# Kernel optimization log

Measured on AMD Instinct MI355X. Metric: run time of the kernel, lower is better.

## Reference

```python
import jax, jax.numpy as jnp
import numpy as np

B, T, C, H = 2, 1024, 768, 12
D = C // H
HID = 4 * C
EPS_YAT = 1e-6
EPS_LN = 1e-6


def yat_dense(x, kernel, bias, alpha):
    # scale = (sqrt(n_out)/log(1+n_out))**alpha
    y = x @ kernel
    dist = (jnp.sum(x * x, axis=-1, keepdims=True)
            + jnp.sum(kernel * kernel, axis=0) - 2.0 * y)
    y = (y * y) / (dist + EPS_YAT)
    if bias is not None:
        y = y + bias
    n = kernel.shape[1]
    scale = (jnp.sqrt(jnp.float32(n)) / jnp.log1p(jnp.float32(n))) ** alpha
    return y * scale


def layernorm(x, scale):
    mu = jnp.mean(x, axis=-1, keepdims=True)
    var = jnp.mean((x - mu) ** 2, axis=-1, keepdims=True)
    return (x - mu) * jax.lax.rsqrt(var + EPS_LN) * scale


def rope_table(seq_len, dim):
    freqs = jnp.exp(jnp.arange(0, dim, 2, dtype=jnp.float32)
                    * (-jnp.log(10000.0) / dim))
    angles = jnp.arange(seq_len, dtype=jnp.float32)[:, None] * freqs[None, :]
    return jnp.concatenate([jnp.cos(angles), jnp.sin(angles)], axis=-1)  # [T, D]


def block_forward(x, mask, p):
    Bc, Tc, Cc = x.shape
    h = layernorm(x, p['ln1_scale'])
    qkv = yat_dense(h, p['w_qkv'], p['b_qkv'], p['a_qkv'])  # [B,T,3C]
    qkv = qkv.reshape(Bc, Tc, 3, H, D)
    q, k, v = qkv[:, :, 0], qkv[:, :, 1], qkv[:, :, 2]      # [B,T,H,D]
    rope = rope_table(Tc, D)[:, None, :]                     # [T,1,D]
    q = q * rope
    k = k * rope
    scale = 1.0 / jnp.sqrt(jnp.float32(D))
    attn = jnp.einsum('bihd,bjhd->bhij', q, k) * scale       # [B,H,T,T]
    attn = jnp.where(mask, attn, jnp.finfo(attn.dtype).min)
    attn = jax.nn.softmax(attn, axis=-1)
    o = jnp.einsum('bhij,bjhd->bihd', attn, v).reshape(Bc, Tc, Cc)
    o = yat_dense(o, p['w_ao'], p['b_ao'], p['a_ao'])
    x = x + o
    h = layernorm(x, p['ln2_scale'])
    gate = yat_dense(h, p['w_fc'], p['b_fc'], p['a_fc'])
    u = yat_dense(h, p['w_gate'], p['b_gate'], p['a_gate'])
    u = jax.nn.gelu(u) * gate
    u = yat_dense(u, p['w_proj'], p['b_proj'], p['a_proj'])
    return x + u


def setup_inputs() -> dict:
    key = jax.random.key(0)
    ks = jax.random.split(key, 8)
    x = jax.random.normal(ks[0], (B, T, C), dtype=jnp.float32)
    mask = jnp.tril(jnp.ones((T, T), dtype=bool))[None, None]  # causal [1,1,T,T]
    w = lambda k, shp: 0.02 * jax.random.normal(k, shp, dtype=jnp.float32)
    return {
        'x': x, 'mask': mask,
        'ln1_scale': jnp.ones((C,), jnp.float32),
        'w_qkv': w(ks[1], (C, 3 * C)), 'b_qkv': jnp.zeros((3 * C,), jnp.float32),
        'a_qkv': jnp.ones((1,), jnp.float32),
        'w_ao': w(ks[2], (C, C)), 'b_ao': jnp.zeros((C,), jnp.float32),
        'a_ao': jnp.ones((1,), jnp.float32),
        'ln2_scale': jnp.ones((C,), jnp.float32),
        'w_fc': w(ks[3], (C, HID)), 'b_fc': jnp.zeros((HID,), jnp.float32),
        'a_fc': jnp.ones((1,), jnp.float32),
        'w_gate': w(ks[4], (C, HID)), 'b_gate': jnp.zeros((HID,), jnp.float32),
        'a_gate': jnp.ones((1,), jnp.float32),
        'w_proj': w(ks[5], (HID, C)), 'b_proj': jnp.zeros((C,), jnp.float32),
        'a_proj': jnp.ones((1,), jnp.float32),
    }


def reference(x, mask, ln1_scale, w_qkv, b_qkv, a_qkv, w_ao, b_ao, a_ao,
              ln2_scale, w_fc, b_fc, a_fc, w_gate, b_gate, a_gate,
              w_proj, b_proj, a_proj):
    p = dict(ln1_scale=ln1_scale, w_qkv=w_qkv, b_qkv=b_qkv, a_qkv=a_qkv,
             w_ao=w_ao, b_ao=b_ao, a_ao=a_ao, ln2_scale=ln2_scale,
             w_fc=w_fc, b_fc=b_fc, a_fc=a_fc, w_gate=w_gate, b_gate=b_gate,
             a_gate=a_gate, w_proj=w_proj, b_proj=b_proj, a_proj=a_proj)
    return block_forward(x, mask, p)
```

## Files before the change

### kernel.cpp

```cpp
#include <hip/hip_runtime.h>
#include <cstdint>

#define DEVFN static __device__ __forceinline__

typedef __bf16 bf16x8 __attribute__((ext_vector_type(8)));
typedef float f32x4 __attribute__((ext_vector_type(4)));
typedef unsigned short us4 __attribute__((ext_vector_type(4)));

DEVFN unsigned short f2bf(float f) {
  unsigned u = __float_as_uint(f);
  u += 0x7fffu + ((u >> 16) & 1u);
  return (unsigned short)(u >> 16);
}
DEVFN float bf2f(unsigned short h) { return __uint_as_float(((unsigned)h) << 16); }
DEVFN void async16(const void* g, void* l) {
  __builtin_amdgcn_global_load_lds((__attribute__((address_space(1))) const void*)g,
                                   (__attribute__((address_space(3))) void*)l, 16, 0, 0);
}
DEVFN float gelu_t(float u) {
  float z = 0.7978845608028654f * (u + 0.044715f * u * u * u);
  float zc = fminf(fmaxf(z, -15.f), 15.f);
  float e = __expf(2.f * zc);
  return u * __fdividef(e, e + 1.f);
}
DEVFN int xcd_swizzle(int lin, int total) {
  return (lin & 7) * (total >> 3) + (lin >> 3);
}

struct PrepArgs {
  float* rope;
  const float* W[5]; unsigned short* Wt[5]; float* cn[5];
  int N[5]; int off[6];
  const float* x; const float* g1s; unsigned short* h1; float* hrow1;
};
__global__ __launch_bounds__(256) void k_prep(PrepArgs a) {
  __shared__ float tile[32][33];
  __shared__ float part[8][32];
  __shared__ float red[12];
  const int bid = blockIdx.x, tid = threadIdx.x;
  if (bid < 256) {
    int g = bid * 256 + tid;
    int t = g >> 6, dd = g & 63, i = dd & 31;
    float fr = __expf(-0.2878231366242558f * (float)i);
    float ang = (float)t * fr;
    a.rope[g] = (dd < 32) ? cosf(ang) : sinf(ang);
  } else if (bid < 9472) {
    int lin = bid - 256;
    int e = 0;
    while (lin >= a.off[e + 1]) ++e;
    int local = lin - a.off[e];
    const int N = a.N[e];
    int nbx = N >> 5;
    int tn = local % nbx, tk = local / nbx;
    const float* W = a.W[e];
    unsigned short* Wt = a.Wt[e];
    float* cn = a.cn[e];
    const int K = (e == 4) ? 3072 : 768;
    int tx = tid & 31, ty = tid >> 5;
    float acc = 0.f;
    #pragma unroll
    for (int j = 0; j < 4; ++j) {
      int r = ty + j * 8;
      float v = W[(long)(tk * 32 + r) * N + tn * 32 + tx];
      tile[r][tx] = v;
      acc += v * v;
    }
    part[ty][tx] = acc;
    __syncthreads();
    #pragma unroll
    for (int j = 0; j < 4; ++j) {
      int rr = ty + j * 8;
      Wt[(long)(tn * 32 + rr) * K + tk * 32 + tx] = f2bf(tile[tx][rr]);
    }
    if (ty == 0) {
      float s = part[0][tx];
      #pragma unroll
      for (int jj = 1; jj < 8; ++jj) s += part[jj][tx];
      atomicAdd(&cn[tn * 32 + tx], s);
    }
  } else {
    int row = bid - 9472;
    const float* xr = a.x + (long)row * 768;
    float v0 = xr[tid], v1 = xr[tid + 256], v2 = xr[tid + 512];
    float s = v0 + v1 + v2;
    float ss = v0 * v0 + v1 * v1 + v2 * v2;
    #pragma unroll
    for (int o = 32; o; o >>= 1) { s += __shfl_xor(s, o); ss += __shfl_xor(ss, o); }
    int wv = tid >> 6;
    if ((tid & 63) == 0) { red[wv] = s; red[wv + 4] = ss; }
    __syncthreads();
    s = red[0] + red[1] + red[2] + red[3];
    ss = red[4] + red[5] + red[6] + red[7];
    float mu = s * (1.f / 768.f);
    float var = ss * (1.f / 768.f) - mu * mu;
    float rs = rsqrtf(var + 1e-6f);
    float h0 = (v0 - mu) * rs * a.g1s[tid];
    float h1 = (v1 - mu) * rs * a.g1s[tid + 256];
    float h2 = (v2 - mu) * rs * a.g1s[tid + 512];
    unsigned short* hr = a.h1 + (long)row * 768;
    hr[tid] = f2bf(h0); hr[tid + 256] = f2bf(h1); hr[tid + 512] = f2bf(h2);
    float p = h0 * h0 + h1 * h1 + h2 * h2;
    #pragma unroll
    for (int o = 32; o; o >>= 1) p += __shfl_xor(p, o);
    if ((tid & 63) == 0) red[8 + wv] = p;
    __syncthreads();
    if (tid == 0) a.hrow1[row] = red[8] + red[9] + red[10] + red[11];
  }
}

__global__ __launch_bounds__(256) void k_ln(const float* __restrict__ x,
    const float* __restrict__ g, unsigned short* __restrict__ h, float* __restrict__ row2) {
  int row = blockIdx.x, tid = threadIdx.x;
  const float* xr = x + (long)row * 768;
  float v0 = xr[tid], v1 = xr[tid + 256], v2 = xr[tid + 512];
  float s = v0 + v1 + v2;
  float ss = v0 * v0 + v1 * v1 + v2 * v2;
  #pragma unroll
  for (int o = 32; o; o >>= 1) { s += __shfl_xor(s, o); ss += __shfl_xor(ss, o); }
  __shared__ float red[12];
  int wv = tid >> 6;
  if ((tid & 63) == 0) { red[wv] = s; red[wv + 4] = ss; }
  __syncthreads();
  s = red[0] + red[1] + red[2] + red[3];
  ss = red[4] + red[5] + red[6] + red[7];
  float mu = s * (1.f / 768.f);
  float var = ss * (1.f / 768.f) - mu * mu;
  float rs = rsqrtf(var + 1e-6f);
  float h0 = (v0 - mu) * rs * g[tid];
  float h1 = (v1 - mu) * rs * g[tid + 256];
  float h2 = (v2 - mu) * rs * g[tid + 512];
  unsigned short* hr = h + (long)row * 768;
  hr[tid] = f2bf(h0); hr[tid + 256] = f2bf(h1); hr[tid + 512] = f2bf(h2);
  float p = h0 * h0 + h1 * h1 + h2 * h2;
  #pragma unroll
  for (int o = 32; o; o >>= 1) p += __shfl_xor(p, o);
  if ((tid & 63) == 0) red[8 + wv] = p;
  __syncthreads();
  if (tid == 0) row2[row] = red[8] + red[9] + red[10] + red[11];
}

constexpr int M_QKV = 0, M_AO = 1, M_PART = 2;

struct GemmArgs {
  const unsigned short* A; const unsigned short* Bt;
  const float* arow2; const float* wcol2; const float* bias; const float* alpha;
  int N; int ks;
  const float* rope;
  unsigned short* qo; unsigned short* ko; unsigned short* vo;
  const float* xf; float* xo;
  unsigned short* partb;
};

template <int MODE, int NI, int NBM, int NBN, int NZ>
__global__ __launch_bounds__(256, 4) void k_gemm(GemmArgs p) {
  __shared__ __align__(16) unsigned short As[3][2048];
  __shared__ __align__(16) unsigned short Bs[3][4096];
  const int tid = threadIdx.x, wave = tid >> 6, lane = tid & 63;
  const int quad = lane >> 4, l = lane & 15;
  constexpr int TOTAL = NBM * NBN * NZ;
  const int g = xcd_swizzle(blockIdx.x, TOTAL);
  const int bm = (g % NBM) * 64;
  const int rest = g / NBM;
  const int bn = (rest % NBN) * 128;
  const int z = rest / NBN;
  const int kb = z * (NI * 32);
  const int ks = p.ks;
  const int wm = (wave & 1) * 32, wn = (wave >> 1) * 64;
  const f32x4 fzero = {0.f, 0.f, 0.f, 0.f};
  f32x4 acc[2][4];
  #pragma unroll
  for (int i = 0; i < 2; ++i)
    #pragma unroll
    for (int j = 0; j < 4; ++j) acc[i][j] = fzero;
  const int sw = (l >> 1) & 3;

  auto stage = [&](int s, int k0) {
    {
      int ci = tid;
      int r = ci >> 2;
      int c = (ci & 3) ^ ((r >> 1) & 3);
      async16(p.A + (long)(bm + r) * ks + kb + k0 + c * 8, &As[s][ci * 8]);
    }
    #pragma unroll
    for (int it = 0; it < 2; ++it) {
      int ci = tid + it * 256;
      int r = ci >> 2;
      int c = (ci & 3) ^ ((r >> 1) & 3);
      async16(p.Bt + (long)(bn + r) * ks + kb + k0 + c * 8, &Bs[s][ci * 8]);
    }
  };
  auto compute = [&](int s) {
    bf16x8 af[2], bfv[4];
    #pragma unroll
    for (int mi = 0; mi < 2; ++mi)
      af[mi] = *(const bf16x8*)&As[s][(wm + mi * 16 + l) * 32 + ((quad ^ sw) * 8)];
    #pragma unroll
    for (int ni = 0; ni < 4; ++ni)
      bfv[ni] = *(const bf16x8*)&Bs[s][(wn + ni * 16 + l) * 32 + ((quad ^ sw) * 8)];
    #pragma unroll
    for (int mi = 0; mi < 2; ++mi)
      #pragma unroll
      for (int ni = 0; ni < 4; ++ni)
        acc[mi][ni] = __builtin_amdgcn_mfma_f32_16x16x32_bf16(af[mi], bfv[ni], acc[mi][ni], 0, 0, 0);
  };
  auto iter = [&](int s, int i) {
    if (i + 1 >= NI) { asm volatile("s_waitcnt vmcnt(0)" ::: "memory"); }
    else             { asm volatile("s_waitcnt vmcnt(3)" ::: "memory"); }
    __builtin_amdgcn_s_barrier();
    asm volatile("" ::: "memory");
    if (i + 2 < NI) stage(s == 0 ? 2 : s - 1, (i + 2) * 32);
    compute(s);
  };

  stage(0, 0);
  stage(1, 32);
  int i = 0;
  while (i < NI) {
    iter(0, i); ++i;
    iter(1, i); ++i;
    iter(2, i); ++i;
  }

  if constexpr (MODE == M_PART) {
    unsigned short* slab = p.partb + (long)z * (2048 * 768);
    #pragma unroll
    for (int ni = 0; ni < 4; ++ni) {
      const int j = bn + wn + ni * 16 + l;
      #pragma unroll
      for (int mi = 0; mi < 2; ++mi) {
        const int i0 = bm + wm + mi * 16 + quad * 4;
        #pragma unroll
        for (int rg = 0; rg < 4; ++rg)
          slab[(long)(i0 + rg) * 768 + j] = f2bf(acc[mi][ni][rg]);
      }
    }
  } else {
    const float al = p.alpha[0];
    const float nn = (float)p.N;
    const float ys = powf(sqrtf(nn) / log1pf(nn), al);
    #pragma unroll
    for (int ni = 0; ni < 4; ++ni) {
      const int j = bn + wn + ni * 16 + l;
      const float w2 = p.wcol2[j];
      const float bj = p.bias[j];
      int s3 = 0, hh = 0, dd = 0;
      if constexpr (MODE == M_QKV) { s3 = j / 768; int rem = j - s3 * 768; hh = rem >> 6; dd = rem & 63; }
      #pragma unroll
      for (int mi = 0; mi < 2; ++mi) {
        const int i0 = bm + wm + mi * 16 + quad * 4;
        float vv[4];
        #pragma unroll
        for (int rg = 0; rg < 4; ++rg) {
          const float y = acc[mi][ni][rg];
          const float dist = p.arow2[i0 + rg] + w2 - 2.f * y + 1e-6f;
          vv[rg] = (__fdividef(y * y, dist) + bj) * ys;
        }
        if constexpr (MODE == M_QKV) {
          int b = i0 >> 10, t0 = i0 & 1023;
          if (s3 == 2) {
            us4 pk = {f2bf(vv[0]), f2bf(vv[1]), f2bf(vv[2]), f2bf(vv[3])};
            *(us4*)&p.vo[((long)(b * 12 + hh) * 64 + dd) * 1024 + t0] = pk;
          } else {
            unsigned short* dst = (s3 == 0) ? p.qo : p.ko;
            #pragma unroll
            for (int rg = 0; rg < 4; ++rg) {
              float ro = p.rope[(t0 + rg) * 64 + dd];
              dst[((long)(b * 12 + hh) * 1024 + t0 + rg) * 64 + dd] = f2bf(vv[rg] * ro);
            }
          }
        } else {
          #pragma unroll
          for (int rg = 0; rg < 4; ++rg) {
            long idx = (long)(i0 + rg) * 768 + j;
            p.xo[idx] = p.xf[idx] + vv[rg];
          }
        }
      }
    }
  }
}

struct EpiArgs {
  const unsigned short* slab; const float* arow2; const float* wcol2;
  const float* bias; const float* alpha; const float* xo; float* outf;
};
__global__ __launch_bounds__(256) void k_proj_epi(EpiArgs p) {
  int g = blockIdx.x * 256 + threadIdx.x;
  int i = g / 192, jv = (g - i * 192) * 4;
  long base = (long)i * 768 + jv;
  f32x4 y = {0.f, 0.f, 0.f, 0.f};
  #pragma unroll
  for (int z = 0; z < 4; ++z) {
    us4 s4 = *(const us4*)(p.slab + (long)z * 1572864 + base);
    #pragma unroll
    for (int c = 0; c < 4; ++c) y[c] += bf2f(s4[c]);
  }
  const float a2 = p.arow2[i];
  const float ys = powf(sqrtf(768.f) / log1pf(768.f), p.alpha[0]);
  f32x4 xo4 = *(const f32x4*)(p.xo + base);
  f32x4 out;
  #pragma unroll
  for (int c = 0; c < 4; ++c) {
    float yy = y[c];
    float dist = a2 + p.wcol2[jv + c] - 2.f * yy + 1e-6f;
    out[c] = xo4[c] + (__fdividef(yy * yy, dist) + p.bias[jv + c]) * ys;
  }
  *(f32x4*)(p.outf + base) = out;
}

struct MlpArgs {
  const unsigned short* A; const unsigned short* Bf; const unsigned short* Bg;
  const float* arow2; const float* w2f; const float* w2g;
  const float* bf; const float* bg; const float* af_; const float* ag_;
  unsigned short* mlp; float* mrow2;
};

__global__ __launch_bounds__(256, 3) void k_mlp(MlpArgs p) {
  constexpr int NI = 24, K = 768;
  __shared__ __align__(16) unsigned short Bfs[3][4096];
  __shared__ __align__(16) unsigned short Bgs[3][4096];
  const int tid = threadIdx.x, wave = tid >> 6, lane = tid & 63;
  const int quad = lane >> 4, l = lane & 15;
  const int g = xcd_swizzle(blockIdx.x, 32 * 24);
  const int bm = (g % 32) * 64, bn = (g / 32) * 128;
  const int wm = (wave & 1) * 32, wn = (wave >> 1) * 64;
  const f32x4 fzero = {0.f, 0.f, 0.f, 0.f};
  f32x4 accf[2][4], accg[2][4];
  #pragma unroll
  for (int i = 0; i < 2; ++i)
    #pragma unroll
    for (int j = 0; j < 4; ++j) { accf[i][j] = fzero; accg[i][j] = fzero; }
  const int sw = (l >> 1) & 3;

  auto stageB = [&](int s, int k0) {
    #pragma unroll
    for (int it = 0; it < 2; ++it) {
      int ci = tid + it * 256;
      int r = ci >> 2;
      int c = (ci & 3) ^ ((r >> 1) & 3);
      async16(p.Bf + (long)(bn + r) * K + k0 + c * 8, &Bfs[s][ci * 8]);
      async16(p.Bg + (long)(bn + r) * K + k0 + c * 8, &Bgs[s][ci * 8]);
    }
  };

  stageB(0, 0);
  stageB(1, 32);
  const unsigned short* Arow0 = p.A + (long)(bm + wm + l) * K + quad * 8;
  const unsigned short* Arow1 = Arow0 + 16 * K;
  for (int i = 0; i < NI; ++i) {
    const int s = i % 3;
    const int k0 = i * 32;
    bf16x8 af0 = *(const bf16x8*)(Arow0 + k0);
    bf16x8 af1 = *(const bf16x8*)(Arow1 + k0);
    if (i + 1 >= NI) { asm volatile("s_waitcnt vmcnt(2)" ::: "memory"); }
    else             { asm volatile("s_waitcnt vmcnt(6)" ::: "memory"); }
    __builtin_amdgcn_s_barrier();
    asm volatile("" ::: "memory");
    if (i + 2 < NI) stageB((i + 2) % 3, (i + 2) * 32);
    bf16x8 bff[4], bfg[4];
    #pragma unroll
    for (int ni = 0; ni < 4; ++ni) {
      bff[ni] = *(const bf16x8*)&Bfs[s][(wn + ni * 16 + l) * 32 + ((quad ^ sw) * 8)];
      bfg[ni] = *(const bf16x8*)&Bgs[s][(wn + ni * 16 + l) * 32 + ((quad ^ sw) * 8)];
    }
    #pragma unroll
    for (int ni = 0; ni < 4; ++ni) {
      accf[0][ni] = __builtin_amdgcn_mfma_f32_16x16x32_bf16(af0, bff[ni], accf[0][ni], 0, 0, 0);
      accg[0][ni] = __builtin_amdgcn_mfma_f32_16x16x32_bf16(af0, bfg[ni], accg[0][ni], 0, 0, 0);
      accf[1][ni] = __builtin_amdgcn_mfma_f32_16x16x32_bf16(af1, bff[ni], accf[1][ni], 0, 0, 0);
      accg[1][ni] = __builtin_amdgcn_mfma_f32_16x16x32_bf16(af1, bfg[ni], accg[1][ni], 0, 0, 0);
    }
  }

  const float ysf = powf(sqrtf(3072.f) / log1pf(3072.f), p.af_[0]);
  const float ysg = powf(sqrtf(3072.f) / log1pf(3072.f), p.ag_[0]);
  float w2f[4], w2g[4], bjf[4], bjg[4]; int js[4];
  #pragma unroll
  for (int ni = 0; ni < 4; ++ni) {
    int j = bn + wn + ni * 16 + l;
    js[ni] = j; w2f[ni] = p.w2f[j]; w2g[ni] = p.w2g[j]; bjf[ni] = p.bf[j]; bjg[ni] = p.bg[j];
  }
  #pragma unroll
  for (int mi = 0; mi < 2; ++mi) {
    #pragma unroll
    for (int rg = 0; rg < 4; ++rg) {
      const int ii = bm + wm + mi * 16 + quad * 4 + rg;
      const float a2 = p.arow2[ii];
      float rsum = 0.f;
      #pragma unroll
      for (int ni = 0; ni < 4; ++ni) {
        float yf = accf[mi][ni][rg];
        float gate = (__fdividef(yf * yf, a2 + w2f[ni] - 2.f * yf + 1e-6f) + bjf[ni]) * ysf;
        float yg = accg[mi][ni][rg];
        float u  = (__fdividef(yg * yg, a2 + w2g[ni] - 2.f * yg + 1e-6f) + bjg[ni]) * ysg;
        float out = gelu_t(u) * gate;
        p.mlp[(long)ii * 3072 + js[ni]] = f2bf(out);
        rsum += out * out;
      }
      #pragma unroll
      for (int o = 8; o; o >>= 1) rsum += __shfl_xor(rsum, o);
      if (l == 0) atomicAdd(&p.mrow2[ii], rsum);
    }
  }
}

__global__ __launch_bounds__(256) void k_attn(const unsigned short* __restrict__ qb,
    const unsigned short* __restrict__ kb, const unsigned short* __restrict__ vb,
    unsigned short* __restrict__ ob, float* __restrict__ orow2) {
  __shared__ __align__(16) unsigned short Qs[4096];
  __shared__ __align__(16) unsigned short Ks[3][4096];
  __shared__ __align__(16) unsigned short Vs[3][4096];
  __shared__ __align__(16) unsigned short Ps[4096];
  const int tid = threadIdx.x, wave = tid >> 6, lane = tid & 63;
  const int quad = lane >> 4, l = lane & 15;
  const int g = xcd_swizzle(blockIdx.x, 16 * 24);
  const int bh = g % 24, qt = 15 - (g / 24);
  const int b = bh / 12, hh = bh % 12;
  const int q0 = qt * 64;
  const f32x4 fzero = {0.f, 0.f, 0.f, 0.f};

  auto stage_kv = [&](int s, int jt) {
    const unsigned short* kg = kb + ((long)bh * 1024 + jt * 64) * 64;
    const unsigned short* vg = vb + (long)bh * 64 * 1024 + jt * 64;
    #pragma unroll
    for (int it = 0; it < 2; ++it) {
      int ci = tid + it * 256;
      int r = ci >> 3;
      int c = (ci & 7) ^ (r & 7);
      async16(kg + (long)r * 64 + c * 8, &Ks[s][ci * 8]);
      async16(vg + (long)r * 1024 + c * 8, &Vs[s][ci * 8]);
    }
  };

  const unsigned short* qg = qb + ((long)bh * 1024 + q0) * 64;
  #pragma unroll
  for (int it = 0; it < 2; ++it) {
    int ci = tid + it * 256;
    int r = ci >> 3;
    int c = (ci & 7) ^ (r & 7);
    async16(qg + (long)r * 64 + c * 8, &Qs[ci * 8]);
  }
  stage_kv(0, 0);
  if (qt >= 1) {
    stage_kv(1, 1);
    asm volatile("s_waitcnt vmcnt(4)" ::: "memory");
  } else {
    asm volatile("s_waitcnt vmcnt(0)" ::: "memory");
  }
  __builtin_amdgcn_s_barrier();
  asm volatile("" ::: "memory");

  bf16x8 aq[2];
  #pragma unroll
  for (int ks = 0; ks < 2; ++ks)
    aq[ks] = *(const bf16x8*)&Qs[(wave * 16 + l) * 64 + (((ks * 4 + quad) ^ (l & 7)) * 8)];

  f32x4 O[4];
  float mi_[4], li[4];
  #pragma unroll
  for (int f = 0; f < 4; ++f) O[f] = fzero;
  #pragma unroll
  for (int r = 0; r < 4; ++r) { mi_[r] = -1e30f; li[r] = 0.f; }

  for (int jt = 0; jt <= qt; ++jt) {
    const int s = jt % 3;
    if (jt > 0) {
      if (jt + 1 <= qt) { asm volatile("s_waitcnt vmcnt(4)" ::: "memory"); }
      else              { asm volatile("s_waitcnt vmcnt(0)" ::: "memory"); }
      __builtin_amdgcn_s_barrier();
      asm volatile("" ::: "memory");
    }
    if (jt + 2 <= qt) stage_kv((jt + 2) % 3, jt + 2);

    f32x4 S[4];
    #pragma unroll
    for (int f = 0; f < 4; ++f) S[f] = fzero;
    #pragma unroll
    for (int ks = 0; ks < 2; ++ks) {
      #pragma unroll
      for (int f = 0; f < 4; ++f) {
        bf16x8 bk = *(const bf16x8*)&Ks[s][(f * 16 + l) * 64 + (((ks * 4 + quad) ^ (l & 7)) * 8)];
        S[f] = __builtin_amdgcn_mfma_f32_16x16x32_bf16(aq[ks], bk, S[f], 0, 0, 0);
      }
    }
    const bool diag = (jt == qt);
    #pragma unroll
    for (int f = 0; f < 4; ++f)
      #pragma unroll
      for (int r = 0; r < 4; ++r) {
        float v = S[f][r] * 0.125f;
        if (diag && (f * 16 + l > wave * 16 + quad * 4 + r)) v = -1e30f;
        S[f][r] = v;
      }
    #pragma unroll
    for (int r = 0; r < 4; ++r) {
      float mx = fmaxf(fmaxf(S[0][r], S[1][r]), fmaxf(S[2][r], S[3][r]));
      #pragma unroll
      for (int o = 8; o; o >>= 1) mx = fmaxf(mx, __shfl_xor(mx, o));
      float mnew = fmaxf(mi_[r], mx);
      float alr = __expf(mi_[r] - mnew);
      float sum = 0.f;
      #pragma unroll
      for (int f = 0; f < 4; ++f) {
        float e = __expf(S[f][r] - mnew);
        S[f][r] = e;
        sum += e;
      }
      #pragma unroll
      for (int o = 8; o; o >>= 1) sum += __shfl_xor(sum, o);
      li[r] = li[r] * alr + sum;
      #pragma unroll
      for (int f = 0; f < 4; ++f) O[f][r] *= alr;
      mi_[r] = mnew;
    }
    #pragma unroll
    for (int f = 0; f < 4; ++f)
      #pragma unroll
      for (int r = 0; r < 4; ++r) {
        int i = quad * 4 + r;
        int j = f * 16 + l;
        int pch = (j >> 3) ^ (i & 7);
        Ps[wave * 1024 + i * 64 + pch * 8 + (j & 7)] = f2bf(S[f][r]);
      }
    #pragma unroll
    for (int ks = 0; ks < 2; ++ks) {
      bf16x8 ap = *(const bf16x8*)&Ps[wave * 1024 + l * 64 + (((ks * 4 + quad) ^ (l & 7)) * 8)];
      #pragma unroll
      for (int f = 0; f < 4; ++f) {
        bf16x8 bv = *(const bf16x8*)&Vs[s][(f * 16 + l) * 64 + (((ks * 4 + quad) ^ (l & 7)) * 8)];
        O[f] = __builtin_amdgcn_mfma_f32_16x16x32_bf16(ap, bv, O[f], 0, 0, 0);
      }
    }
  }
  float inv[4];
  #pragma unroll
  for (int r = 0; r < 4; ++r) inv[r] = __fdividef(1.f, li[r]);
  #pragma unroll
  for (int f = 0; f < 4; ++f)
    #pragma unroll
    for (int r = 0; r < 4; ++r) {
      int t = q0 + wave * 16 + quad * 4 + r;
      int dd = f * 16 + l;
      ob[((long)(b * 1024 + t) * 12 + hh) * 64 + dd] = f2bf(O[f][r] * inv[r]);
    }
  #pragma unroll
  for (int r = 0; r < 4; ++r) {
    float rsum = 0.f;
    #pragma unroll
    for (int f = 0; f < 4; ++f) { float v = O[f][r] * inv[r]; rsum += v * v; }
    #pragma unroll
    for (int o = 8; o; o >>= 1) rsum += __shfl_xor(rsum, o);
    if (l == 0) {
      int t = q0 + wave * 16 + quad * 4 + r;
      atomicAdd(&orow2[b * 1024 + t], rsum);
    }
  }
}

extern "C" void kernel_launch(void* const* d_in, const int* in_sizes, int n_in,
                              void* d_out, int out_size, void* d_ws, size_t ws_size,
                              hipStream_t stream) {
  (void)in_sizes; (void)n_in; (void)out_size;
  char* w = (char*)d_ws;
  size_t off = 0;
  auto alloc = [&](size_t bytes) -> void* {
    void* p = w + off;
    off = (off + bytes + 255) & ~(size_t)255;
    return p;
  };
  float* rope            = (float*)alloc(65536 * 4);
  unsigned short* wtqkv  = (unsigned short*)alloc((size_t)2304 * 768 * 2);
  unsigned short* wtao   = (unsigned short*)alloc((size_t)768 * 768 * 2);
  unsigned short* wtfc   = (unsigned short*)alloc((size_t)3072 * 768 * 2);
  unsigned short* wtgate = (unsigned short*)alloc((size_t)3072 * 768 * 2);
  unsigned short* wtproj = (unsigned short*)alloc((size_t)768 * 3072 * 2);
  float* zeroed          = (float*)alloc(14080 * 4);
  unsigned short* h1     = (unsigned short*)alloc((size_t)2048 * 768 * 2);
  float* hrow1           = (float*)alloc(2048 * 4);
  unsigned short* qbuf   = (unsigned short*)alloc((size_t)2048 * 768 * 2);
  unsigned short* kbuf   = (unsigned short*)alloc((size_t)2048 * 768 * 2);
  unsigned short* vbuf   = (unsigned short*)alloc((size_t)2048 * 768 * 2);
  unsigned short* obuf   = (unsigned short*)alloc((size_t)2048 * 768 * 2);
  float* xo              = (float*)alloc((size_t)2048 * 768 * 4);
  unsigned short* h2     = (unsigned short*)alloc((size_t)2048 * 768 * 2);
  float* hrow2           = (float*)alloc(2048 * 4);
  unsigned short* mlp    = (unsigned short*)alloc((size_t)2048 * 3072 * 2);
  unsigned short* slabs  = (unsigned short*)alloc((size_t)4 * 2048 * 768 * 2);
  if (off > ws_size) return;

  float* wcol2  = zeroed;
  float* orow2  = zeroed + 9984;
  float* mrow2  = zeroed + 9984 + 2048;
  float* c_qkv  = wcol2 + 0;
  float* c_ao   = wcol2 + 2304;
  float* c_fc   = wcol2 + 3072;
  float* c_gate = wcol2 + 6144;
  float* c_proj = wcol2 + 9216;

  const float* xin = (const float*)d_in[0];

  hipMemsetAsync(zeroed, 0, 14080 * 4, stream);

  PrepArgs pa;
  pa.rope = rope;
  pa.W[0] = (const float*)d_in[3];  pa.Wt[0] = wtqkv;  pa.cn[0] = c_qkv;  pa.N[0] = 2304;
  pa.W[1] = (const float*)d_in[6];  pa.Wt[1] = wtao;   pa.cn[1] = c_ao;   pa.N[1] = 768;
  pa.W[2] = (const float*)d_in[10]; pa.Wt[2] = wtfc;   pa.cn[2] = c_fc;   pa.N[2] = 3072;
  pa.W[3] = (const float*)d_in[13]; pa.Wt[3] = wtgate; pa.cn[3] = c_gate; pa.N[3] = 3072;
  pa.W[4] = (const float*)d_in[16]; pa.Wt[4] = wtproj; pa.cn[4] = c_proj; pa.N[4] = 768;
  pa.off[0] = 0; pa.off[1] = 1728; pa.off[2] = 2304; pa.off[3] = 4608;
  pa.off[4] = 6912; pa.off[5] = 9216;
  pa.x = xin; pa.g1s = (const float*)d_in[2]; pa.h1 = h1; pa.hrow1 = hrow1;
  k_prep<<<11520, 256, 0, stream>>>(pa);

  GemmArgs gq = {};
  gq.A = h1; gq.Bt = wtqkv; gq.arow2 = hrow1; gq.wcol2 = c_qkv;
  gq.bias = (const float*)d_in[4]; gq.alpha = (const float*)d_in[5];
  gq.N = 2304; gq.ks = 768;
  gq.rope = rope; gq.qo = qbuf; gq.ko = kbuf; gq.vo = vbuf;
  k_gemm<M_QKV, 24, 32, 18, 1><<<576, 256, 0, stream>>>(gq);

  k_attn<<<384, 256, 0, stream>>>(qbuf, kbuf, vbuf, obuf, orow2);

  GemmArgs ga = {};
  ga.A = obuf; ga.Bt = wtao; ga.arow2 = orow2; ga.wcol2 = c_ao;
  ga.bias = (const float*)d_in[7]; ga.alpha = (const float*)d_in[8];
  ga.N = 768; ga.ks = 768;
  ga.xf = xin; ga.xo = xo;
  k_gemm<M_AO, 24, 32, 6, 1><<<192, 256, 0, stream>>>(ga);

  k_ln<<<2048, 256, 0, stream>>>(xo, (const float*)d_in[9], h2, hrow2);

  MlpArgs gm = {};
  gm.A = h2; gm.Bf = wtfc; gm.Bg = wtgate; gm.arow2 = hrow2;
  gm.w2f = c_fc; gm.w2g = c_gate;
  gm.bf = (const float*)d_in[11]; gm.bg = (const float*)d_in[14];
  gm.af_ = (const float*)d_in[12]; gm.ag_ = (const float*)d_in[15];
  gm.mlp = mlp; gm.mrow2 = mrow2;
  k_mlp<<<768, 256, 0, stream>>>(gm);

  GemmArgs gp = {};
  gp.A = mlp; gp.Bt = wtproj;
  gp.N = 768; gp.ks = 3072;
  gp.partb = slabs;
  k_gemm<M_PART, 24, 32, 6, 4><<<768, 256, 0, stream>>>(gp);

  EpiArgs ge = {};
  ge.slab = slabs; ge.arow2 = mrow2; ge.wcol2 = c_proj;
  ge.bias = (const float*)d_in[17]; ge.alpha = (const float*)d_in[18];
  ge.xo = xo; ge.outf = (float*)d_out;
  k_proj_epi<<<1536, 256, 0, stream>>>(ge);
}
```

Before: 276.7 us.

## Use 32x32 MFMA 128x128 tiles for MLP and proj split-K GEMMs

Replaces the MLP fc/gate kernel and the projection split-K GEMM with new kernels that use 128x128 block tiles and 32x32x16 bf16 MFMA instructions, staging A through LDS in the MLP kernel too. The projection GEMM now splits K eight ways instead of four, and the epilogue reduces eight bf16 partial slabs. The aim is more data reuse per block and fewer LDS reads per MFMA. The cost is more register pressure and lower occupancy (launch bounds 2-3), fewer blocks for the MLP kernel, and twice as much partial-slab traffic in the epilogue.

```diff
diff --git a/kernel.cpp b/kernel.cpp
--- a/kernel.cpp
+++ b/kernel.cpp
@@ -5,6 +5,7 @@
 
 typedef __bf16 bf16x8 __attribute__((ext_vector_type(8)));
 typedef float f32x4 __attribute__((ext_vector_type(4)));
+typedef float f32x16 __attribute__((ext_vector_type(16)));
 typedef unsigned short us4 __attribute__((ext_vector_type(4)));
 
 DEVFN unsigned short f2bf(float f) {
@@ -26,6 +27,7 @@
 DEVFN int xcd_swizzle(int lin, int total) {
   return (lin & 7) * (total >> 3) + (lin >> 3);
 }
+DEVFN int row32(int r, int lhalf) { return (r & 3) + 8 * (r >> 2) + 4 * lhalf; }
 
 struct PrepArgs {
   float* rope;
@@ -139,7 +141,7 @@
   if (tid == 0) row2[row] = red[8] + red[9] + red[10] + red[11];
 }
 
-constexpr int M_QKV = 0, M_AO = 1, M_PART = 2;
+constexpr int M_QKV = 0, M_AO = 1;
 
 struct GemmArgs {
   const unsigned short* A; const unsigned short* Bt;
@@ -148,22 +150,18 @@
   const float* rope;
   unsigned short* qo; unsigned short* ko; unsigned short* vo;
   const float* xf; float* xo;
-  unsigned short* partb;
 };
 
-template <int MODE, int NI, int NBM, int NBN, int NZ>
+template <int MODE, int NI, int NBM, int NBN>
 __global__ __launch_bounds__(256, 4) void k_gemm(GemmArgs p) {
   __shared__ __align__(16) unsigned short As[3][2048];
   __shared__ __align__(16) unsigned short Bs[3][4096];
   const int tid = threadIdx.x, wave = tid >> 6, lane = tid & 63;
   const int quad = lane >> 4, l = lane & 15;
-  constexpr int TOTAL = NBM * NBN * NZ;
+  constexpr int TOTAL = NBM * NBN;
   const int g = xcd_swizzle(blockIdx.x, TOTAL);
   const int bm = (g % NBM) * 64;
-  const int rest = g / NBM;
-  const int bn = (rest % NBN) * 128;
-  const int z = rest / NBN;
-  const int kb = z * (NI * 32);
+  const int bn = (g / NBM) * 128;
   const int ks = p.ks;
   const int wm = (wave & 1) * 32, wn = (wave >> 1) * 64;
   const f32x4 fzero = {0.f, 0.f, 0.f, 0.f};
@@ -179,14 +177,14 @@
       int ci = tid;
       int r = ci >> 2;
       int c = (ci & 3) ^ ((r >> 1) & 3);
-      async16(p.A + (long)(bm + r) * ks + kb + k0 + c * 8, &As[s][ci * 8]);
+      async16(p.A + (long)(bm + r) * ks + k0 + c * 8, &As[s][ci * 8]);
     }
     #pragma unroll
     for (int it = 0; it < 2; ++it) {
       int ci = tid + it * 256;
       int r = ci >> 2;
       int c = (ci & 3) ^ ((r >> 1) & 3);
-      async16(p.Bt + (long)(bn + r) * ks + kb + k0 + c * 8, &Bs[s][ci * 8]);
+      async16(p.Bt + (long)(bn + r) * ks + k0 + c * 8, &Bs[s][ci * 8]);
     }
   };
   auto compute = [&](int s) {
@@ -221,61 +219,245 @@
     iter(2, i); ++i;
   }
 
-  if constexpr (MODE == M_PART) {
-    unsigned short* slab = p.partb + (long)z * (2048 * 768);
-    #pragma unroll
-    for (int ni = 0; ni < 4; ++ni) {
-      const int j = bn + wn + ni * 16 + l;
-      #pragma unroll
-      for (int mi = 0; mi < 2; ++mi) {
-        const int i0 = bm + wm + mi * 16 + quad * 4;
-        #pragma unroll
-        for (int rg = 0; rg < 4; ++rg)
-          slab[(long)(i0 + rg) * 768 + j] = f2bf(acc[mi][ni][rg]);
-      }
-    }
-  } else {
-    const float al = p.alpha[0];
-    const float nn = (float)p.N;
-    const float ys = powf(sqrtf(nn) / log1pf(nn), al);
-    #pragma unroll
-    for (int ni = 0; ni < 4; ++ni) {
-      const int j = bn + wn + ni * 16 + l;
-      const float w2 = p.wcol2[j];
-      const float bj = p.bias[j];
-      int s3 = 0, hh = 0, dd = 0;
-      if constexpr (MODE == M_QKV) { s3 = j / 768; int rem = j - s3 * 768; hh = rem >> 6; dd = rem & 63; }
-      #pragma unroll
-      for (int mi = 0; mi < 2; ++mi) {
-        const int i0 = bm + wm + mi * 16 + quad * 4;
-        float vv[4];
+  const float al = p.alpha[0];
+  const float nn = (float)p.N;
+  const float ys = powf(sqrtf(nn) / log1pf(nn), al);
+  #pragma unroll
+  for (int ni = 0; ni < 4; ++ni) {
+    const int j = bn + wn + ni * 16 + l;
+    const float w2 = p.wcol2[j];
+    const float bj = p.bias[j];
+    int s3 = 0, hh = 0, dd = 0;
+    if constexpr (MODE == M_QKV) { s3 = j / 768; int rem = j - s3 * 768; hh = rem >> 6; dd = rem & 63; }
+    #pragma unroll
+    for (int mi = 0; mi < 2; ++mi) {
+      const int i0 = bm + wm + mi * 16 + quad * 4;
+      float vv[4];
+      #pragma unroll
+      for (int rg = 0; rg < 4; ++rg) {
+        const float y = acc[mi][ni][rg];
+        const float dist = p.arow2[i0 + rg] + w2 - 2.f * y + 1e-6f;
+        vv[rg] = (__fdividef(y * y, dist) + bj) * ys;
+      }
+      if constexpr (MODE == M_QKV) {
+        int b = i0 >> 10, t0 = i0 & 1023;
+        if (s3 == 2) {
+          us4 pk = {f2bf(vv[0]), f2bf(vv[1]), f2bf(vv[2]), f2bf(vv[3])};
+          *(us4*)&p.vo[((long)(b * 12 + hh) * 64 + dd) * 1024 + t0] = pk;
+        } else {
+          unsigned short* dst = (s3 == 0) ? p.qo : p.ko;
+          #pragma unroll
+          for (int rg = 0; rg < 4; ++rg) {
+            float ro = p.rope[(t0 + rg) * 64 + dd];
+            dst[((long)(b * 12 + hh) * 1024 + t0 + rg) * 64 + dd] = f2bf(vv[rg] * ro);
+          }
+        }
+      } else {
         #pragma unroll
         for (int rg = 0; rg < 4; ++rg) {
-          const float y = acc[mi][ni][rg];
-          const float dist = p.arow2[i0 + rg] + w2 - 2.f * y + 1e-6f;
-          vv[rg] = (__fdividef(y * y, dist) + bj) * ys;
+          long idx = (long)(i0 + rg) * 768 + j;
+          p.xo[idx] = p.xf[idx] + vv[rg];
         }
-        if constexpr (MODE == M_QKV) {
-          int b = i0 >> 10, t0 = i0 & 1023;
-          if (s3 == 2) {
-            us4 pk = {f2bf(vv[0]), f2bf(vv[1]), f2bf(vv[2]), f2bf(vv[3])};
-            *(us4*)&p.vo[((long)(b * 12 + hh) * 64 + dd) * 1024 + t0] = pk;
-          } else {
-            unsigned short* dst = (s3 == 0) ? p.qo : p.ko;
-            #pragma unroll
-            for (int rg = 0; rg < 4; ++rg) {
-              float ro = p.rope[(t0 + rg) * 64 + dd];
-              dst[((long)(b * 12 + hh) * 1024 + t0 + rg) * 64 + dd] = f2bf(vv[rg] * ro);
-            }
-          }
-        } else {
-          #pragma unroll
-          for (int rg = 0; rg < 4; ++rg) {
-            long idx = (long)(i0 + rg) * 768 + j;
-            p.xo[idx] = p.xf[idx] + vv[rg];
-          }
+      }
+    }
+  }
+}
+
+
+struct PartArgs {
+  const unsigned short* A; const unsigned short* Bt;
+  unsigned short* partb;
+};
+__global__ __launch_bounds__(256, 3) void k_part32(PartArgs p) {
+  constexpr int NI = 12, KS = 3072;
+  __shared__ __align__(16) unsigned short As[3][4096];
+  __shared__ __align__(16) unsigned short Bs[3][4096];
+  const int tid = threadIdx.x, wave = tid >> 6, lane = tid & 63;
+  const int l5 = lane >> 5, l31 = lane & 31;
+  const int g = xcd_swizzle(blockIdx.x, 768);
+  const int bm = (g % 16) * 128;
+  const int rest = g / 16;
+  const int bn = (rest % 6) * 128;
+  const int z = rest / 6;
+  const int kb = z * 384;
+  const int wm = (wave & 1) * 64, wn = (wave >> 1) * 64;
+  f32x16 acc[2][2];
+  #pragma unroll
+  for (int i = 0; i < 2; ++i)
+    #pragma unroll
+    for (int j = 0; j < 2; ++j)
+      #pragma unroll
+      for (int c = 0; c < 16; ++c) acc[i][j][c] = 0.f;
+
+  auto stage = [&](int s, int k0) {
+    #pragma unroll
+    for (int it = 0; it < 2; ++it) {
+      int ci = tid + it * 256;
+      int r = ci >> 2;
+      int c = (ci & 3) ^ (r & 3);
+      async16(p.A + (long)(bm + r) * KS + kb + k0 + c * 8, &As[s][ci * 8]);
+      async16(p.Bt + (long)(bn + r) * KS + kb + k0 + c * 8, &Bs[s][ci * 8]);
+    }
+  };
+  auto compute = [&](int s) {
+    #pragma unroll
+    for (int kh = 0; kh < 2; ++kh) {
+      bf16x8 a[2], b[2];
+      #pragma unroll
+      for (int mi = 0; mi < 2; ++mi) {
+        int r = wm + mi * 32 + l31;
+        a[mi] = *(const bf16x8*)&As[s][r * 32 + (((kh * 2 + l5) ^ (r & 3)) * 8)];
+      }
+      #pragma unroll
+      for (int ni = 0; ni < 2; ++ni) {
+        int r = wn + ni * 32 + l31;
+        b[ni] = *(const bf16x8*)&Bs[s][r * 32 + (((kh * 2 + l5) ^ (r & 3)) * 8)];
+      }
+      #pragma unroll
+      for (int mi = 0; mi < 2; ++mi)
+        #pragma unroll
+        for (int ni = 0; ni < 2; ++ni)
+          acc[mi][ni] = __builtin_amdgcn_mfma_f32_32x32x16_bf16(a[mi], b[ni], acc[mi][ni], 0, 0, 0);
+    }
+  };
+  auto iter = [&](int s, int i) {
+    if (i + 1 >= NI) { asm volatile("s_waitcnt vmcnt(0)" ::: "memory"); }
+    else             { asm volatile("s_waitcnt vmcnt(4)" ::: "memory"); }
+    __builtin_amdgcn_s_barrier();
+    asm volatile("" ::: "memory");
+    if (i + 2 < NI) stage(s == 0 ? 2 : s - 1, (i + 2) * 32);
+    compute(s);
+  };
+
+  stage(0, 0);
+  stage(1, 32);
+  int i = 0;
+  while (i < NI) {
+    iter(0, i); ++i;
+    iter(1, i); ++i;
+    iter(2, i); ++i;
+  }
+
+  unsigned short* slab = p.partb + (long)z * (2048 * 768);
+  #pragma unroll
+  for (int mi = 0; mi < 2; ++mi)
+    #pragma unroll
+    for (int ni = 0; ni < 2; ++ni) {
+      const int j = bn + wn + ni * 32 + l31;
+      #pragma unroll
+      for (int rg = 0; rg < 16; ++rg) {
+        const int ii = bm + wm + mi * 32 + row32(rg, l5);
+        slab[(long)ii * 768 + j] = f2bf(acc[mi][ni][rg]);
+      }
+    }
+}
+
+struct MlpArgs {
+  const unsigned short* A; const unsigned short* Bf; const unsigned short* Bg;
+  const float* arow2; const float* w2f; const float* w2g;
+  const float* bf; const float* bg; const float* af_; const float* ag_;
+  unsigned short* mlp; float* mrow2;
+};
+__global__ __launch_bounds__(256, 2) void k_mlp32(MlpArgs p) {
+  constexpr int NI = 24, K = 768;
+  __shared__ __align__(16) unsigned short As[3][4096];
+  __shared__ __align__(16) unsigned short Bfs[3][4096];
+  __shared__ __align__(16) unsigned short Bgs[3][4096];
+  const int tid = threadIdx.x, wave = tid >> 6, lane = tid & 63;
+  const int l5 = lane >> 5, l31 = lane & 31;
+  const int g = xcd_swizzle(blockIdx.x, 384);
+  const int bm = (g % 16) * 128, bn = (g / 16) * 128;
+  const int wm = (wave & 1) * 64, wn = (wave >> 1) * 64;
+  f32x16 accf[2][2], accg[2][2];
+  #pragma unroll
+  for (int i = 0; i < 2; ++i)
+    #pragma unroll
+    for (int j = 0; j < 2; ++j)
+      #pragma unroll
+      for (int c = 0; c < 16; ++c) { accf[i][j][c] = 0.f; accg[i][j][c] = 0.f; }
+
+  auto stage = [&](int s, int k0) {
+    #pragma unroll
+    for (int it = 0; it < 2; ++it) {
+      int ci = tid + it * 256;
+      int r = ci >> 2;
+      int c = (ci & 3) ^ (r & 3);
+      async16(p.A  + (long)(bm + r) * K + k0 + c * 8, &As[s][ci * 8]);
+      async16(p.Bf + (long)(bn + r) * K + k0 + c * 8, &Bfs[s][ci * 8]);
+      async16(p.Bg + (long)(bn + r) * K + k0 + c * 8, &Bgs[s][ci * 8]);
+    }
+  };
+  auto compute = [&](int s) {
+    #pragma unroll
+    for (int kh = 0; kh < 2; ++kh) {
+      bf16x8 a[2], bfv[2], bgv[2];
+      #pragma unroll
+      for (int mi = 0; mi < 2; ++mi) {
+        int r = wm + mi * 32 + l31;
+        a[mi] = *(const bf16x8*)&As[s][r * 32 + (((kh * 2 + l5) ^ (r & 3)) * 8)];
+      }
+      #pragma unroll
+      for (int ni = 0; ni < 2; ++ni) {
+        int r = wn + ni * 32 + l31;
+        int off = r * 32 + (((kh * 2 + l5) ^ (r & 3)) * 8);
+        bfv[ni] = *(const bf16x8*)&Bfs[s][off];
+        bgv[ni] = *(const bf16x8*)&Bgs[s][off];
+      }
+      #pragma unroll
+      for (int mi = 0; mi < 2; ++mi)
+        #pragma unroll
+        for (int ni = 0; ni < 2; ++ni) {
+          accf[mi][ni] = __builtin_amdgcn_mfma_f32_32x32x16_bf16(a[mi], bfv[ni], accf[mi][ni], 0, 0, 0);
+          accg[mi][ni] = __builtin_amdgcn_mfma_f32_32x32x16_bf16(a[mi], bgv[ni], accg[mi][ni], 0, 0, 0);
         }
-      }
+    }
+  };
+  auto iter = [&](int s, int i) {
+    if (i + 1 >= NI) { asm volatile("s_waitcnt vmcnt(0)" ::: "memory"); }
+    else             { asm volatile("s_waitcnt vmcnt(6)" ::: "memory"); }
+    __builtin_amdgcn_s_barrier();
+    asm volatile("" ::: "memory");
+    if (i + 2 < NI) stage(s == 0 ? 2 : s - 1, (i + 2) * 32);
+    compute(s);
+  };
+
+  stage(0, 0);
+  stage(1, 32);
+  int i = 0;
+  while (i < NI) {
+    iter(0, i); ++i;
+    iter(1, i); ++i;
+    iter(2, i); ++i;
+  }
+
+  const float ysf = powf(sqrtf(3072.f) / log1pf(3072.f), p.af_[0]);
+  const float ysg = powf(sqrtf(3072.f) / log1pf(3072.f), p.ag_[0]);
+  float w2f[2], w2g[2], bjf[2], bjg[2]; int js[2];
+  #pragma unroll
+  for (int ni = 0; ni < 2; ++ni) {
+    int j = bn + wn + ni * 32 + l31;
+    js[ni] = j; w2f[ni] = p.w2f[j]; w2g[ni] = p.w2g[j]; bjf[ni] = p.bf[j]; bjg[ni] = p.bg[j];
+  }
+  #pragma unroll
+  for (int mi = 0; mi < 2; ++mi) {
+    #pragma unroll
+    for (int rg = 0; rg < 16; ++rg) {
+      const int ii = bm + wm + mi * 32 + row32(rg, l5);
+      const float a2 = p.arow2[ii];
+      float rsum = 0.f;
+      #pragma unroll
+      for (int ni = 0; ni < 2; ++ni) {
+        float yf = accf[mi][ni][rg];
+        float gate = (__fdividef(yf * yf, a2 + w2f[ni] - 2.f * yf + 1e-6f) + bjf[ni]) * ysf;
+        float yg = accg[mi][ni][rg];
+        float u  = (__fdividef(yg * yg, a2 + w2g[ni] - 2.f * yg + 1e-6f) + bjg[ni]) * ysg;
+        float out = gelu_t(u) * gate;
+        p.mlp[(long)ii * 3072 + js[ni]] = f2bf(out);
+        rsum += out * out;
+      }
+      #pragma unroll
+      for (int o = 16; o; o >>= 1) rsum += __shfl_xor(rsum, o);
+      if (l31 == 0) atomicAdd(&p.mrow2[ii], rsum);
     }
   }
 }
@@ -290,7 +472,7 @@
   long base = (long)i * 768 + jv;
   f32x4 y = {0.f, 0.f, 0.f, 0.f};
   #pragma unroll
-  for (int z = 0; z < 4; ++z) {
+  for (int z = 0; z < 8; ++z) {
     us4 s4 = *(const us4*)(p.slab + (long)z * 1572864 + base);
     #pragma unroll
     for (int c = 0; c < 4; ++c) y[c] += bf2f(s4[c]);
@@ -306,102 +488,6 @@
     out[c] = xo4[c] + (__fdividef(yy * yy, dist) + p.bias[jv + c]) * ys;
   }
   *(f32x4*)(p.outf + base) = out;
-}
-
-struct MlpArgs {
-  const unsigned short* A; const unsigned short* Bf; const unsigned short* Bg;
-  const float* arow2; const float* w2f; const float* w2g;
-  const float* bf; const float* bg; const float* af_; const float* ag_;
-  unsigned short* mlp; float* mrow2;
-};
-
-__global__ __launch_bounds__(256, 3) void k_mlp(MlpArgs p) {
-  constexpr int NI = 24, K = 768;
-  __shared__ __align__(16) unsigned short Bfs[3][4096];
-  __shared__ __align__(16) unsigned short Bgs[3][4096];
-  const int tid = threadIdx.x, wave = tid >> 6, lane = tid & 63;
-  const int quad = lane >> 4, l = lane & 15;
-  const int g = xcd_swizzle(blockIdx.x, 32 * 24);
-  const int bm = (g % 32) * 64, bn = (g / 32) * 128;
-  const int wm = (wave & 1) * 32, wn = (wave >> 1) * 64;
-  const f32x4 fzero = {0.f, 0.f, 0.f, 0.f};
-  f32x4 accf[2][4], accg[2][4];
-  #pragma unroll
-  for (int i = 0; i < 2; ++i)
-    #pragma unroll
-    for (int j = 0; j < 4; ++j) { accf[i][j] = fzero; accg[i][j] = fzero; }
-  const int sw = (l >> 1) & 3;
-
-  auto stageB = [&](int s, int k0) {
-    #pragma unroll
-    for (int it = 0; it < 2; ++it) {
-      int ci = tid + it * 256;
-      int r = ci >> 2;
-      int c = (ci & 3) ^ ((r >> 1) & 3);
-      async16(p.Bf + (long)(bn + r) * K + k0 + c * 8, &Bfs[s][ci * 8]);
-      async16(p.Bg + (long)(bn + r) * K + k0 + c * 8, &Bgs[s][ci * 8]);
-    }
-  };
-
-  stageB(0, 0);
-  stageB(1, 32);
-  const unsigned short* Arow0 = p.A + (long)(bm + wm + l) * K + quad * 8;
-  const unsigned short* Arow1 = Arow0 + 16 * K;
-  for (int i = 0; i < NI; ++i) {
-    const int s = i % 3;
-    const int k0 = i * 32;
-    bf16x8 af0 = *(const bf16x8*)(Arow0 + k0);
-    bf16x8 af1 = *(const bf16x8*)(Arow1 + k0);
-    if (i + 1 >= NI) { asm volatile("s_waitcnt vmcnt(2)" ::: "memory"); }
-    else             { asm volatile("s_waitcnt vmcnt(6)" ::: "memory"); }
-    __builtin_amdgcn_s_barrier();
-    asm volatile("" ::: "memory");
-    if (i + 2 < NI) stageB((i + 2) % 3, (i + 2) * 32);
-    bf16x8 bff[4], bfg[4];
-    #pragma unroll
-    for (int ni = 0; ni < 4; ++ni) {
-      bff[ni] = *(const bf16x8*)&Bfs[s][(wn + ni * 16 + l) * 32 + ((quad ^ sw) * 8)];
-      bfg[ni] = *(const bf16x8*)&Bgs[s][(wn + ni * 16 + l) * 32 + ((quad ^ sw) * 8)];
-    }
-    #pragma unroll
-    for (int ni = 0; ni < 4; ++ni) {
-      accf[0][ni] = __builtin_amdgcn_mfma_f32_16x16x32_bf16(af0, bff[ni], accf[0][ni], 0, 0, 0);
-      accg[0][ni] = __builtin_amdgcn_mfma_f32_16x16x32_bf16(af0, bfg[ni], accg[0][ni], 0, 0, 0);
-      accf[1][ni] = __builtin_amdgcn_mfma_f32_16x16x32_bf16(af1, bff[ni], accf[1][ni], 0, 0, 0);
-      accg[1][ni] = __builtin_amdgcn_mfma_f32_16x16x32_bf16(af1, bfg[ni], accg[1][ni], 0, 0, 0);
-    }
-  }
-
-  const float ysf = powf(sqrtf(3072.f) / log1pf(3072.f), p.af_[0]);
-  const float ysg = powf(sqrtf(3072.f) / log1pf(3072.f), p.ag_[0]);
-  float w2f[4], w2g[4], bjf[4], bjg[4]; int js[4];
-  #pragma unroll
-  for (int ni = 0; ni < 4; ++ni) {
-    int j = bn + wn + ni * 16 + l;
-    js[ni] = j; w2f[ni] = p.w2f[j]; w2g[ni] = p.w2g[j]; bjf[ni] = p.bf[j]; bjg[ni] = p.bg[j];
-  }
-  #pragma unroll
-  for (int mi = 0; mi < 2; ++mi) {
-    #pragma unroll
-    for (int rg = 0; rg < 4; ++rg) {
-      const int ii = bm + wm + mi * 16 + quad * 4 + rg;
-      const float a2 = p.arow2[ii];
-      float rsum = 0.f;
-      #pragma unroll
-      for (int ni = 0; ni < 4; ++ni) {
-        float yf = accf[mi][ni][rg];
-        float gate = (__fdividef(yf * yf, a2 + w2f[ni] - 2.f * yf + 1e-6f) + bjf[ni]) * ysf;
-        float yg = accg[mi][ni][rg];
-        float u  = (__fdividef(yg * yg, a2 + w2g[ni] - 2.f * yg + 1e-6f) + bjg[ni]) * ysg;
-        float out = gelu_t(u) * gate;
-        p.mlp[(long)ii * 3072 + js[ni]] = f2bf(out);
-        rsum += out * out;
-      }
-      #pragma unroll
-      for (int o = 8; o; o >>= 1) rsum += __shfl_xor(rsum, o);
-      if (l == 0) atomicAdd(&p.mrow2[ii], rsum);
-    }
-  }
 }
 
 __global__ __launch_bounds__(256) void k_attn(const unsigned short* __restrict__ qb,
@@ -585,7 +671,7 @@
   unsigned short* h2     = (unsigned short*)alloc((size_t)2048 * 768 * 2);
   float* hrow2           = (float*)alloc(2048 * 4);
   unsigned short* mlp    = (unsigned short*)alloc((size_t)2048 * 3072 * 2);
-  unsigned short* slabs  = (unsigned short*)alloc((size_t)4 * 2048 * 768 * 2);
+  unsigned short* slabs  = (unsigned short*)alloc((size_t)8 * 2048 * 768 * 2);
   if (off > ws_size) return;
 
   float* wcol2  = zeroed;
@@ -618,7 +704,7 @@
   gq.bias = (const float*)d_in[4]; gq.alpha = (const float*)d_in[5];
   gq.N = 2304; gq.ks = 768;
   gq.rope = rope; gq.qo = qbuf; gq.ko = kbuf; gq.vo = vbuf;
-  k_gemm<M_QKV, 24, 32, 18, 1><<<576, 256, 0, stream>>>(gq);
+  k_gemm<M_QKV, 24, 32, 18><<<576, 256, 0, stream>>>(gq);
 
   k_attn<<<384, 256, 0, stream>>>(qbuf, kbuf, vbuf, obuf, orow2);
 
@@ -627,7 +713,7 @@
   ga.bias = (const float*)d_in[7]; ga.alpha = (const float*)d_in[8];
   ga.N = 768; ga.ks = 768;
   ga.xf = xin; ga.xo = xo;
-  k_gemm<M_AO, 24, 32, 6, 1><<<192, 256, 0, stream>>>(ga);
+  k_gemm<M_AO, 24, 32, 6><<<192, 256, 0, stream>>>(ga);
 
   k_ln<<<2048, 256, 0, stream>>>(xo, (const float*)d_in[9], h2, hrow2);
 
@@ -637,13 +723,11 @@
   gm.bf = (const float*)d_in[11]; gm.bg = (const float*)d_in[14];
   gm.af_ = (const float*)d_in[12]; gm.ag_ = (const float*)d_in[15];
   gm.mlp = mlp; gm.mrow2 = mrow2;
-  k_mlp<<<768, 256, 0, stream>>>(gm);
-
-  GemmArgs gp = {};
-  gp.A = mlp; gp.Bt = wtproj;
-  gp.N = 768; gp.ks = 3072;
-  gp.partb = slabs;
-  k_gemm<M_PART, 24, 32, 6, 4><<<768, 256, 0, stream>>>(gp);
+  k_mlp32<<<384, 256, 0, stream>>>(gm);
+
+  PartArgs gp = {};
+  gp.A = mlp; gp.Bt = wtproj; gp.partb = slabs;
+  k_part32<<<768, 256, 0, stream>>>(gp);
 
   EpiArgs ge = {};
   ge.slab = slabs; ge.arow2 = mrow2; ge.wcol2 = c_proj;
```

Measured after the change: 285.8 us. +3.3%, slower.
